# Optimization experiments

Hardware: AMD Instinct MI355X
Metric: run time of the kernel (lower is better)

The kernel has to match this reference:

```python
import jax, jax.numpy as jnp
import numpy as np

N_EPOCH = 1000
LR = 1e-3      # torch.optim.Adam defaults
BETA1 = 0.9
BETA2 = 0.999
EPS = 1e-8


def setup_inputs() -> dict:
    key = jax.random.key(0)
    k1, k2 = jax.random.split(key)
    H = jax.random.normal(k1, (128, 2048), dtype=jnp.float32)        # test activations [n_test, d]
    H_train = jax.random.normal(k2, (2048, 2048), dtype=jnp.float32)  # corpus activations [n_train, d]
    return {"H": H, "H_train": H_train}


def reference(H, H_train):
    n_test, n_train = H.shape[0], H_train.shape[0]

    def loss_fn(P):
        W = jax.nn.softmax(P, axis=-1)              # [n_test, n_train]
        H_approx = W @ H_train                       # einsum ij,jk->ik
        return jnp.sum((H_approx - H) ** 2)

    grad_fn = jax.grad(loss_fn)

    P0 = jnp.zeros((n_test, n_train), dtype=H.dtype)
    m0 = jnp.zeros_like(P0)
    v0 = jnp.zeros_like(P0)

    def adam_step(carry, t):
        P, m, v = carry
        g = grad_fn(P)
        m = BETA1 * m + (1.0 - BETA1) * g
        v = BETA2 * v + (1.0 - BETA2) * (g * g)
        m_hat = m / (1.0 - BETA1 ** t)
        v_hat = v / (1.0 - BETA2 ** t)
        P = P - LR * m_hat / (jnp.sqrt(v_hat) + EPS)
        return (P, m, v), None

    steps = jnp.arange(1, N_EPOCH + 1, dtype=H.dtype)  # 1-based Adam step count
    (P, _, _), _ = jax.lax.scan(adam_step, (P0, m0, v0), steps)
    return jax.nn.softmax(P, axis=-1)
```

## Files before the change

kernel.cpp:

```cpp
#include <hip/hip_runtime.h>
#include <math.h>

#define DN 2048
#define NT 128

constexpr float LR    = 1e-3f;
constexpr float BETA1 = 0.9f;
constexpr float BETA2 = 0.999f;
constexpr float EPSA  = 1e-8f;

__device__ __forceinline__ float f4get(const float4& v, int k) {
    return k == 0 ? v.x : (k == 1 ? v.y : (k == 2 ? v.z : v.w));
}

template <bool TRANSB>
__global__ __launch_bounds__(512)
void matpart_kernel(const float* __restrict__ L, const float* __restrict__ R,
                    float* __restrict__ out_parts)
{
    __shared__ __align__(16) float Ws[128][36];
    __shared__ __align__(16) float At[32][36];
    const int j0    = blockIdx.x * 32;
    const int kbase = blockIdx.y * 512;
    const int tx = threadIdx.x;
    const int cg = tx & 7;
    const int rg = tx >> 3;
    float4 acc0 = {0.f, 0.f, 0.f, 0.f};
    float4 acc1 = {0.f, 0.f, 0.f, 0.f};

    for (int s = 0; s < 16; ++s) {
        const int k0 = kbase + s * 32;
        {
            int idx = tx;
            #pragma unroll
            for (int rr = 0; rr < 2; ++rr) {
                const int row = idx >> 3, f = idx & 7;
                const float4 wv = *(const float4*)&L[row * DN + k0 + 4 * f];
                *(float4*)&Ws[row][4 * f] = wv;
                idx += 512;
            }
            if (tx < 256) {
                if (!TRANSB) {
                    const int kk = tx >> 3, f = tx & 7;
                    const float4 av = *(const float4*)&R[(size_t)(k0 + kk) * DN + j0 + 4 * f];
                    *(float4*)&At[kk][4 * f] = av;
                } else {
                    const int c = tx >> 3, f = tx & 7;
                    const float4 av = *(const float4*)&R[(size_t)(j0 + c) * DN + k0 + 4 * f];
                    At[4 * f + 0][c] = av.x;
                    At[4 * f + 1][c] = av.y;
                    At[4 * f + 2][c] = av.z;
                    At[4 * f + 3][c] = av.w;
                }
            }
        }
        __syncthreads();
        #pragma unroll
        for (int kq = 0; kq < 8; ++kq) {
            const float4 w0 = *(const float4*)&Ws[rg][4 * kq];
            const float4 w1 = *(const float4*)&Ws[rg + 64][4 * kq];
            #pragma unroll
            for (int kk = 0; kk < 4; ++kk) {
                const float4 av = *(const float4*)&At[4 * kq + kk][4 * cg];
                const float wa = f4get(w0, kk);
                const float wb = f4get(w1, kk);
                acc0.x += wa * av.x; acc0.y += wa * av.y;
                acc0.z += wa * av.z; acc0.w += wa * av.w;
                acc1.x += wb * av.x; acc1.y += wb * av.y;
                acc1.z += wb * av.z; acc1.w += wb * av.w;
            }
        }
        __syncthreads();
    }
    float* op = out_parts + (size_t)blockIdx.y * (NT * DN);
    *(float4*)&op[rg * DN + j0 + 4 * cg] = acc0;
    *(float4*)&op[(rg + 64) * DN + j0 + 4 * cg] = acc1;
}

__global__ __launch_bounds__(256)
void gram_kernel(const float* __restrict__ Ht, float* __restrict__ A)
{
    __shared__ __align__(16) float Ti[64][36];
    __shared__ __align__(16) float Tj[64][36];
    const int i0 = blockIdx.x * 64, j0 = blockIdx.y * 64;
    const int tx = threadIdx.x;
    const int ti = tx & 15;
    const int tj = tx >> 4;
    float4 acc[4];
    #pragma unroll
    for (int a = 0; a < 4; ++a) acc[a] = {0.f, 0.f, 0.f, 0.f};

    for (int s = 0; s < 64; ++s) {
        const int k0 = s * 32;
        {
            int idx = tx;
            #pragma unroll
            for (int rr = 0; rr < 2; ++rr) {
                const int row = idx >> 3, f = idx & 7;
                *(float4*)&Ti[row][4 * f] = *(const float4*)&Ht[(size_t)(i0 + row) * DN + k0 + 4 * f];
                *(float4*)&Tj[row][4 * f] = *(const float4*)&Ht[(size_t)(j0 + row) * DN + k0 + 4 * f];
                idx += 256;
            }
        }
        __syncthreads();
        #pragma unroll
        for (int kq = 0; kq < 8; ++kq) {
            float4 iv[4], jv[4];
            #pragma unroll
            for (int a = 0; a < 4; ++a) iv[a] = *(const float4*)&Ti[ti + 16 * a][4 * kq];
            #pragma unroll
            for (int b = 0; b < 4; ++b) jv[b] = *(const float4*)&Tj[4 * tj + b][4 * kq];
            #pragma unroll
            for (int kk = 0; kk < 4; ++kk) {
                #pragma unroll
                for (int a = 0; a < 4; ++a) {
                    const float wa = f4get(iv[a], kk);
                    acc[a].x += wa * f4get(jv[0], kk);
                    acc[a].y += wa * f4get(jv[1], kk);
                    acc[a].z += wa * f4get(jv[2], kk);
                    acc[a].w += wa * f4get(jv[3], kk);
                }
            }
        }
        __syncthreads();
    }
    #pragma unroll
    for (int a = 0; a < 4; ++a)
        *(float4*)&A[(size_t)(i0 + ti + 16 * a) * DN + j0 + 4 * tj] = acc[a];
}

__global__ void sumB_kernel(const float* __restrict__ parts, float* __restrict__ Bm)
{
    const int idx = (blockIdx.x * 256 + threadIdx.x) * 4;
    float4 a = *(const float4*)&parts[idx];
    const float4 b = *(const float4*)&parts[(size_t)NT * DN + idx];
    const float4 c = *(const float4*)&parts[(size_t)2 * NT * DN + idx];
    const float4 d = *(const float4*)&parts[(size_t)3 * NT * DN + idx];
    a.x += b.x; a.x += c.x; a.x += d.x;
    a.y += b.y; a.y += c.y; a.y += d.y;
    a.z += b.z; a.z += c.z; a.z += d.z;
    a.w += b.w; a.w += c.w; a.w += d.w;
    *(float4*)&Bm[idx] = a;
}

__global__ void init_kernel(float* __restrict__ P, float* __restrict__ M,
                            float* __restrict__ V, float* __restrict__ W)
{
    const int idx = (blockIdx.x * 256 + threadIdx.x) * 4;
    const float4 z = {0.f, 0.f, 0.f, 0.f};
    const float u = 1.f / (float)DN;
    const float4 uu = {u, u, u, u};
    *(float4*)&P[idx] = z;
    *(float4*)&M[idx] = z;
    *(float4*)&V[idx] = z;
    *(float4*)&W[idx] = uu;
}

__device__ __forceinline__ float blk_sum(float x) {
    #pragma unroll
    for (int o = 32; o > 0; o >>= 1) x += __shfl_down(x, o);
    __shared__ float r[4];
    const int tx = threadIdx.x;
    if ((tx & 63) == 0) r[tx >> 6] = x;
    __syncthreads();
    x = (r[0] + r[1]) + (r[2] + r[3]);
    __syncthreads();
    return x;
}

__device__ __forceinline__ float blk_max(float x) {
    #pragma unroll
    for (int o = 32; o > 0; o >>= 1) x = fmaxf(x, __shfl_down(x, o));
    __shared__ float r[4];
    const int tx = threadIdx.x;
    if ((tx & 63) == 0) r[tx >> 6] = x;
    __syncthreads();
    x = fmaxf(fmaxf(r[0], r[1]), fmaxf(r[2], r[3]));
    __syncthreads();
    return x;
}

__global__ __launch_bounds__(256)
void adam_kernel(const float* __restrict__ parts, const float* __restrict__ Bm,
                 float* __restrict__ W, float* __restrict__ P,
                 float* __restrict__ M, float* __restrict__ V,
                 const float bc1, const float bc2)
{
    const int i = blockIdx.x;
    const int tx = threadIdx.x;
    const int base = i * DN + tx * 8;

    float G8[8], W8[8], P8[8], M8[8], V8[8], E8[8];
    {
        float4 s0 = {0.f, 0.f, 0.f, 0.f}, s1 = {0.f, 0.f, 0.f, 0.f};
        #pragma unroll
        for (int p = 0; p < 4; ++p) {
            const float4 x = *(const float4*)&parts[(size_t)p * (NT * DN) + base];
            const float4 y = *(const float4*)&parts[(size_t)p * (NT * DN) + base + 4];
            s0.x += x.x; s0.y += x.y; s0.z += x.z; s0.w += x.w;
            s1.x += y.x; s1.y += y.y; s1.z += y.z; s1.w += y.w;
        }
        const float4 b0 = *(const float4*)&Bm[base];
        const float4 b1 = *(const float4*)&Bm[base + 4];
        G8[0] = 2.f * (s0.x - b0.x); G8[1] = 2.f * (s0.y - b0.y);
        G8[2] = 2.f * (s0.z - b0.z); G8[3] = 2.f * (s0.w - b0.w);
        G8[4] = 2.f * (s1.x - b1.x); G8[5] = 2.f * (s1.y - b1.y);
        G8[6] = 2.f * (s1.z - b1.z); G8[7] = 2.f * (s1.w - b1.w);
    }
    *(float4*)&W8[0] = *(const float4*)&W[base];
    *(float4*)&W8[4] = *(const float4*)&W[base + 4];

    float sp = 0.f;
    #pragma unroll
    for (int e = 0; e < 8; ++e) sp += W8[e] * G8[e];
    const float srow = blk_sum(sp);

    *(float4*)&P8[0] = *(const float4*)&P[base];
    *(float4*)&P8[4] = *(const float4*)&P[base + 4];
    *(float4*)&M8[0] = *(const float4*)&M[base];
    *(float4*)&M8[4] = *(const float4*)&M[base + 4];
    *(float4*)&V8[0] = *(const float4*)&V[base];
    *(float4*)&V8[4] = *(const float4*)&V[base + 4];

    float mx = -1e30f;
    #pragma unroll
    for (int e = 0; e < 8; ++e) {
        const float g  = W8[e] * (G8[e] - srow);
        const float m_ = BETA1 * M8[e] + (1.f - BETA1) * g;
        const float v_ = BETA2 * V8[e] + (1.f - BETA2) * g * g;
        M8[e] = m_; V8[e] = v_;
        const float mh = m_ * bc1;
        const float vh = v_ * bc2;
        const float pn = P8[e] - LR * mh / (sqrtf(vh) + EPSA);
        P8[e] = pn;
        mx = fmaxf(mx, pn);
    }
    mx = blk_max(mx);

    float es = 0.f;
    #pragma unroll
    for (int e = 0; e < 8; ++e) { E8[e] = expf(P8[e] - mx); es += E8[e]; }
    const float sig = blk_sum(es);
    #pragma unroll
    for (int e = 0; e < 8; ++e) W8[e] = E8[e] / sig;

    *(float4*)&W[base]     = *(const float4*)&W8[0];
    *(float4*)&W[base + 4] = *(const float4*)&W8[4];
    *(float4*)&P[base]     = *(const float4*)&P8[0];
    *(float4*)&P[base + 4] = *(const float4*)&P8[4];
    *(float4*)&M[base]     = *(const float4*)&M8[0];
    *(float4*)&M[base + 4] = *(const float4*)&M8[4];
    *(float4*)&V[base]     = *(const float4*)&V8[0];
    *(float4*)&V[base + 4] = *(const float4*)&V8[4];
}

extern "C" void kernel_launch(void* const* d_in, const int* in_sizes, int n_in,
                              void* d_out, int out_size, void* d_ws, size_t ws_size,
                              hipStream_t stream)
{
    const float* H  = (const float*)d_in[0];
    const float* Ht = (const float*)d_in[1];

    float* ws = (float*)d_ws;
    float* A     = ws;
    float* Bm    = A  + (size_t)DN * DN;
    float* P     = Bm + (size_t)NT * DN;
    float* M     = P  + (size_t)NT * DN;
    float* V     = M  + (size_t)NT * DN;
    float* W     = V  + (size_t)NT * DN;
    float* parts = W  + (size_t)NT * DN;

    gram_kernel<<<dim3(32, 32), 256, 0, stream>>>(Ht, A);
    matpart_kernel<true><<<dim3(64, 4), 512, 0, stream>>>(H, Ht, parts);
    sumB_kernel<<<256, 256, 0, stream>>>(parts, Bm);
    init_kernel<<<256, 256, 0, stream>>>(P, M, V, W);

    double b1t = 1.0, b2t = 1.0;
    for (int t = 1; t <= 1000; ++t) {
        b1t *= 0.9; b2t *= 0.999;
        matpart_kernel<false><<<dim3(64, 4), 512, 0, stream>>>(W, A, parts);
        const float bc1 = (float)(1.0 / (1.0 - b1t));
        const float bc2 = (float)(1.0 / (1.0 - b2t));
        adam_kernel<<<NT, 256, 0, stream>>>(parts, Bm, W, P, M, V, bc1, bc2);
    }

    hipMemcpyAsync(d_out, W, (size_t)NT * DN * sizeof(float),
                   hipMemcpyDeviceToDevice, stream);
}
```

Measured before the change: 32.02 ms.

## Replace per-step W·A matmul with wide-column split-K kernel using wave-uniform W rows

The per-iteration product of the softmax weights with the Gram matrix gets its own kernel. Each block stages a 128x256 slab of A in LDS, and each wave computes 8 rows by 256 columns, reading its W rows with wave-uniform addresses so they can be broadcast. The K dimension is now split 8 ways instead of 4, and the Adam kernel sums 8 partial buffers. The aim is more arithmetic per LDS load and less repeated staging of W. In exchange, the partial-sum buffer and its reduction traffic double, and the large LDS footprint limits each CU to one block.

```diff
diff --git a/kernel.cpp b/kernel.cpp
--- a/kernel.cpp
+++ b/kernel.cpp
@@ -3,6 +3,11 @@
 
 #define DN 2048
 #define NT 128
+
+#define KB    8
+#define KLEN  256
+#define CB    256
+#define RB    32
 
 constexpr float LR    = 1e-3f;
 constexpr float BETA1 = 0.9f;
@@ -13,10 +18,73 @@
     return k == 0 ? v.x : (k == 1 ? v.y : (k == 2 ? v.z : v.w));
 }
 
-template <bool TRANSB>
+__global__ __launch_bounds__(256)
+void wa_kernel(const float* __restrict__ W, const float* __restrict__ A,
+               float* __restrict__ parts)
+{
+    __shared__ __align__(16) float At[KLEN / 2][CB];
+    const int colb  = blockIdx.x * CB;
+    const int rowb  = blockIdx.y * RB;
+    const int kb    = blockIdx.z;
+    const int kbase = kb * KLEN;
+    const int tx    = threadIdx.x;
+    const int lane  = tx & 63;
+    const int wid   = __builtin_amdgcn_readfirstlane(tx >> 6);
+    const int row0  = rowb + wid * 8;
+
+    const float* wrow[8];
+    #pragma unroll
+    for (int r = 0; r < 8; ++r)
+        wrow[r] = W + (size_t)(row0 + r) * DN + kbase;
+
+    float4 acc[8];
+    #pragma unroll
+    for (int r = 0; r < 8; ++r) acc[r] = {0.f, 0.f, 0.f, 0.f};
+
+    for (int half = 0; half < 2; ++half) {
+        __syncthreads();
+        {
+            const float* src = A + (size_t)(kbase + half * (KLEN / 2)) * DN + colb;
+            #pragma unroll 8
+            for (int it = 0; it < 32; ++it) {
+                const int f  = it * 256 + tx;
+                const int kr = f >> 6;
+                const int c4 = f & 63;
+                *(float4*)&At[kr][c4 * 4] =
+                    *(const float4*)&src[(size_t)kr * DN + c4 * 4];
+            }
+        }
+        __syncthreads();
+
+        const int hb = half * (KLEN / 2);
+        #pragma unroll 4
+        for (int kc = 0; kc < 32; ++kc) {
+            float4 wv[8];
+            #pragma unroll
+            for (int r = 0; r < 8; ++r)
+                wv[r] = *(const float4*)(wrow[r] + hb + 4 * kc);
+            #pragma unroll
+            for (int kk = 0; kk < 4; ++kk) {
+                const float4 av = *(const float4*)&At[4 * kc + kk][lane * 4];
+                #pragma unroll
+                for (int r = 0; r < 8; ++r) {
+                    const float wk = f4get(wv[r], kk);
+                    acc[r].x += wk * av.x; acc[r].y += wk * av.y;
+                    acc[r].z += wk * av.z; acc[r].w += wk * av.w;
+                }
+            }
+        }
+    }
+
+    float* op = parts + (size_t)kb * (NT * DN);
+    #pragma unroll
+    for (int r = 0; r < 8; ++r)
+        *(float4*)&op[(size_t)(row0 + r) * DN + colb + lane * 4] = acc[r];
+}
+
 __global__ __launch_bounds__(512)
-void matpart_kernel(const float* __restrict__ L, const float* __restrict__ R,
-                    float* __restrict__ out_parts)
+void bpart_kernel(const float* __restrict__ L, const float* __restrict__ R,
+                  float* __restrict__ out_parts)
 {
     __shared__ __align__(16) float Ws[128][36];
     __shared__ __align__(16) float At[32][36];
@@ -40,18 +108,12 @@
                 idx += 512;
             }
             if (tx < 256) {
-                if (!TRANSB) {
-                    const int kk = tx >> 3, f = tx & 7;
-                    const float4 av = *(const float4*)&R[(size_t)(k0 + kk) * DN + j0 + 4 * f];
-                    *(float4*)&At[kk][4 * f] = av;
-                } else {
-                    const int c = tx >> 3, f = tx & 7;
-                    const float4 av = *(const float4*)&R[(size_t)(j0 + c) * DN + k0 + 4 * f];
-                    At[4 * f + 0][c] = av.x;
-                    At[4 * f + 1][c] = av.y;
-                    At[4 * f + 2][c] = av.z;
-                    At[4 * f + 3][c] = av.w;
-                }
+                const int c = tx >> 3, f = tx & 7;
+                const float4 av = *(const float4*)&R[(size_t)(j0 + c) * DN + k0 + 4 * f];
+                At[4 * f + 0][c] = av.x;
+                At[4 * f + 1][c] = av.y;
+                At[4 * f + 2][c] = av.z;
+                At[4 * f + 3][c] = av.w;
             }
         }
         __syncthreads();
@@ -194,7 +256,7 @@
     {
         float4 s0 = {0.f, 0.f, 0.f, 0.f}, s1 = {0.f, 0.f, 0.f, 0.f};
         #pragma unroll
-        for (int p = 0; p < 4; ++p) {
+        for (int p = 0; p < KB; ++p) {
             const float4 x = *(const float4*)&parts[(size_t)p * (NT * DN) + base];
             const float4 y = *(const float4*)&parts[(size_t)p * (NT * DN) + base + 4];
             s0.x += x.x; s0.y += x.y; s0.z += x.z; s0.w += x.w;
@@ -271,14 +333,14 @@
     float* parts = W  + (size_t)NT * DN;
 
     gram_kernel<<<dim3(32, 32), 256, 0, stream>>>(Ht, A);
-    matpart_kernel<true><<<dim3(64, 4), 512, 0, stream>>>(H, Ht, parts);
+    bpart_kernel<<<dim3(64, 4), 512, 0, stream>>>(H, Ht, parts);
     sumB_kernel<<<256, 256, 0, stream>>>(parts, Bm);
     init_kernel<<<256, 256, 0, stream>>>(P, M, V, W);
 
     double b1t = 1.0, b2t = 1.0;
     for (int t = 1; t <= 1000; ++t) {
         b1t *= 0.9; b2t *= 0.999;
-        matpart_kernel<false><<<dim3(64, 4), 512, 0, stream>>>(W, A, parts);
+        wa_kernel<<<dim3(DN / CB, NT / RB, KB), 256, 0, stream>>>(W, A, parts);
         const float bc1 = (float)(1.0 / (1.0 - b1t));
         const float bc2 = (float)(1.0 / (1.0 - b2t));
         adam_kernel<<<NT, 256, 0, stream>>>(parts, Bm, W, P, M, V, bc1, bc2);
```

After: 46.33 ms. 44.7% more time.
